# Kernel optimization log

Hardware: AMD Instinct MI355X
Metric: run time of the kernel (lower is better)

Reference implementation:

```python
import jax, jax.numpy as jnp
import numpy as np

D_MODEL = 1024


def setup_inputs() -> dict:
    key = jax.random.key(0)
    ks = jax.random.split(key, 11)
    B, S, D = 4, 2048, D_MODEL
    scale = 1.0 / np.sqrt(D)
    inp = {
        "query": jax.random.normal(ks[0], (B, S, D), dtype=jnp.float32),
        "key": jax.random.normal(ks[1], (B, S, D), dtype=jnp.float32),
        "value": jax.random.normal(ks[2], (B, S, D), dtype=jnp.float32),
        # nn.Linear weights stored torch-style as [out, in]; y = x @ W.T + b
        "Wq": jax.random.normal(ks[3], (D, D), dtype=jnp.float32) * scale,
        "bq": jnp.zeros((D,), dtype=jnp.float32),
        "Wk": jax.random.normal(ks[4], (D, D), dtype=jnp.float32) * scale,
        "bk": jnp.zeros((D,), dtype=jnp.float32),
        "Wv": jax.random.normal(ks[5], (D, D), dtype=jnp.float32) * scale,
        "bv": jnp.zeros((D,), dtype=jnp.float32),
        "Wo": jax.random.normal(ks[6], (D, D), dtype=jnp.float32) * scale,
        "bo": jnp.zeros((D,), dtype=jnp.float32),
    }
    return inp


def reference(query, key, value, Wq, bq, Wk, bk, Wv, bv, Wo, bo):
    d_model = query.shape[-1]
    q = jnp.einsum("bsd,ed->bse", query, Wq) + bq  # q_proj
    k = jnp.einsum("bsd,ed->bse", key, Wk) + bk    # k_proj
    v = jnp.einsum("bsd,ed->bse", value, Wv) + bv  # v_proj
    # scores scaled by sqrt(d_model) (single head: full d_model, per original code)
    scores = jnp.einsum("bqe,bke->bqk", q, k) / jnp.sqrt(jnp.asarray(d_model, q.dtype))
    attn = jax.nn.softmax(scores, axis=-1)
    # dropout is identity in eval mode
    out = jnp.einsum("bqk,bke->bqe", attn, v)
    out = jnp.einsum("bqe,fe->bqf", out, Wo) + bo  # out_proj
    return out
```

## Files before the change

kernel.cpp:

```cpp
#include <hip/hip_runtime.h>
#include <stdint.h>


typedef __bf16  bf16x8 __attribute__((ext_vector_type(8)));
typedef float   f32x4  __attribute__((ext_vector_type(4)));
typedef unsigned int u32x4 __attribute__((ext_vector_type(4)));

__device__ __forceinline__ unsigned short bf16_rne(float f) {
  unsigned int u = __builtin_bit_cast(unsigned int, f);
  u += 0x7FFFu + ((u >> 16) & 1u);
  return (unsigned short)(u >> 16);
}
__device__ __forceinline__ unsigned int pack2(float a, float b) {
  return (unsigned int)bf16_rne(a) | ((unsigned int)bf16_rne(b) << 16);
}
__device__ __forceinline__ void async16(const unsigned short* g, unsigned short* l) {
  __builtin_amdgcn_global_load_lds(
      (const __attribute__((address_space(1))) unsigned int*)g,
      (__attribute__((address_space(3))) unsigned int*)l,
      16, 0, 0);
}

#define FENCE() asm volatile("" ::: "memory")
#define BAR()   __builtin_amdgcn_s_barrier()

#define MFMA_ __builtin_amdgcn_mfma_f32_16x16x32_bf16

#define T1_REMAP() \
  const int nx   = gridDim.x, ny = gridDim.y; \
  const int nwg  = nx * ny * gridDim.z; \
  const int orig = (blockIdx.z * ny + blockIdx.y) * nx + blockIdx.x; \
  const int xcd  = orig & 7, loc = orig >> 3; \
  const int qq   = nwg >> 3, rr = nwg & 7; \
  const int w    = (xcd < rr ? xcd * (qq + 1) : rr * (qq + 1) + (xcd - rr) * qq) + loc; \
  const int bxi  = w % nx; \
  const int byi  = (w / nx) % ny; \
  const int bzi  = w / (nx * ny);

template<int OUT_F32>
__global__ __launch_bounds__(512, 1) void gemm256(
    const unsigned short* __restrict__ A, const unsigned short* __restrict__ B,
    void* __restrict__ Cp,
    int K, int lda, int ldb, int ldc,
    long sAz, long sBz, long sCz, long sBiasZ,
    float scale, const float* __restrict__ bias, int bias_mode)
{
  __shared__ unsigned short lds[2 * 32768];

  T1_REMAP();

  const int tid  = threadIdx.x;
  const int lane = tid & 63;
  const int wid  = tid >> 6;
  const int bm   = byi * 256;
  const int bn   = bxi * 256;
  const long z   = bzi;

  const unsigned short* Az = A + z * sAz;
  const unsigned short* Bz = B + z * sBz;

  const int wm  = wid >> 2;
  const int wn  = wid & 3;
  const int al  = lane & 15;
  const int ah  = lane >> 4;
  const int al7 = lane & 7;

  const int swz = ((lane & 7) ^ ((lane >> 3) & 7)) << 3;
  const unsigned short* Apt = Az + (long)(bm + wid * 32 + (lane >> 3)) * lda + swz;
  const unsigned short* Bpt = Bz + (long)(bn + wid * 32 + (lane >> 3)) * ldb + swz;
  const long a8 = (long)lda * 8, b8 = (long)ldb * 8;

#define SALL(kt, stg) { \
    const unsigned short* pa_ = Apt + ((long)(kt) << 6); \
    const unsigned short* pb_ = Bpt + ((long)(kt) << 6); \
    async16(pa_,          (stg) + wid * 2048);        \
    async16(pa_ + a8,     (stg) + wid * 2048 + 512);  \
    async16(pa_ + 2 * a8, (stg) + wid * 2048 + 1024); \
    async16(pa_ + 3 * a8, (stg) + wid * 2048 + 1536); \
    async16(pb_,          (stg) + 16384 + wid * 2048);        \
    async16(pb_ + b8,     (stg) + 16384 + wid * 2048 + 512);  \
    async16(pb_ + 2 * b8, (stg) + 16384 + wid * 2048 + 1024); \
    async16(pb_ + 3 * b8, (stg) + 16384 + wid * 2048 + 1536); }

#define LDA2(v0, v1, mm) { const int r_ = (wm * 128 + (mm) * 16 + al) * 64; \
    v0 = *(const bf16x8*)&as[r_ + ((ah ^ al7) << 3)]; \
    v1 = *(const bf16x8*)&as[r_ + (((4 | ah) ^ al7) << 3)]; }
#define LDB2(v0, v1, nn) { const int r_ = (wn * 64 + (nn) * 16 + al) * 64; \
    v0 = *(const bf16x8*)&bs[r_ + ((ah ^ al7) << 3)]; \
    v1 = *(const bf16x8*)&bs[r_ + (((4 | ah) ^ al7) << 3)]; }
#define MM2(mi, ni, av0, av1, bv0, bv1) { \
    acc[mi][ni] = MFMA_(av0, bv0, acc[mi][ni], 0, 0, 0); \
    acc[mi][ni] = MFMA_(av1, bv1, acc[mi][ni], 0, 0, 0); }

  f32x4 acc[8][4] = {};
  const int nkt = K >> 6;

  SALL(0, lds);

  int cur = 0;
  for (int t = 0; t < nkt; ++t) {
    asm volatile("s_waitcnt vmcnt(0)" ::: "memory");
    BAR(); FENCE();

    const unsigned short* as  = lds + cur * 32768;
    const unsigned short* bs  = as + 16384;
    unsigned short*       stg = lds + (cur ^ 1) * 32768;

    if (t + 1 < nkt) SALL(t + 1, stg);

    bf16x8 a0k0, a0k1, a1k0, a1k1, a2k0, a2k1, a3k0, a3k1;
    bf16x8 b0k0, b0k1, b1k0, b1k1, b2k0, b2k1, b3k0, b3k1;

    LDA2(a0k0, a0k1, 0); LDA2(a1k0, a1k1, 1); LDA2(a2k0, a2k1, 2); LDA2(a3k0, a3k1, 3);
    LDB2(b0k0, b0k1, 0); LDB2(b1k0, b1k1, 1);
    FENCE(); BAR();
    __builtin_amdgcn_s_setprio(1);
    MM2(0,0, a0k0,a0k1, b0k0,b0k1); MM2(1,0, a1k0,a1k1, b0k0,b0k1);
    MM2(2,0, a2k0,a2k1, b0k0,b0k1); MM2(3,0, a3k0,a3k1, b0k0,b0k1);
    MM2(0,1, a0k0,a0k1, b1k0,b1k1); MM2(1,1, a1k0,a1k1, b1k0,b1k1);
    MM2(2,1, a2k0,a2k1, b1k0,b1k1); MM2(3,1, a3k0,a3k1, b1k0,b1k1);
    __builtin_amdgcn_s_setprio(0);
    BAR(); FENCE();

    LDB2(b2k0, b2k1, 2); LDB2(b3k0, b3k1, 3);
    FENCE(); BAR();
    __builtin_amdgcn_s_setprio(1);
    MM2(0,2, a0k0,a0k1, b2k0,b2k1); MM2(1,2, a1k0,a1k1, b2k0,b2k1);
    MM2(2,2, a2k0,a2k1, b2k0,b2k1); MM2(3,2, a3k0,a3k1, b2k0,b2k1);
    MM2(0,3, a0k0,a0k1, b3k0,b3k1); MM2(1,3, a1k0,a1k1, b3k0,b3k1);
    MM2(2,3, a2k0,a2k1, b3k0,b3k1); MM2(3,3, a3k0,a3k1, b3k0,b3k1);
    __builtin_amdgcn_s_setprio(0);
    BAR(); FENCE();

    LDA2(a0k0, a0k1, 4); LDA2(a1k0, a1k1, 5); LDA2(a2k0, a2k1, 6); LDA2(a3k0, a3k1, 7);
    FENCE(); BAR();
    __builtin_amdgcn_s_setprio(1);
    MM2(4,0, a0k0,a0k1, b0k0,b0k1); MM2(5,0, a1k0,a1k1, b0k0,b0k1);
    MM2(6,0, a2k0,a2k1, b0k0,b0k1); MM2(7,0, a3k0,a3k1, b0k0,b0k1);
    MM2(4,1, a0k0,a0k1, b1k0,b1k1); MM2(5,1, a1k0,a1k1, b1k0,b1k1);
    MM2(6,1, a2k0,a2k1, b1k0,b1k1); MM2(7,1, a3k0,a3k1, b1k0,b1k1);
    __builtin_amdgcn_s_setprio(0);
    BAR(); FENCE();

    __builtin_amdgcn_s_setprio(1);
    MM2(4,2, a0k0,a0k1, b2k0,b2k1); MM2(5,2, a1k0,a1k1, b2k0,b2k1);
    MM2(6,2, a2k0,a2k1, b2k0,b2k1); MM2(7,2, a3k0,a3k1, b2k0,b2k1);
    MM2(4,3, a0k0,a0k1, b3k0,b3k1); MM2(5,3, a1k0,a1k1, b3k0,b3k1);
    MM2(6,3, a2k0,a2k1, b3k0,b3k1); MM2(7,3, a3k0,a3k1, b3k0,b3k1);
    __builtin_amdgcn_s_setprio(0);

    cur ^= 1;
  }

  #pragma unroll
  for (int m = 0; m < 8; ++m) {
    #pragma unroll
    for (int n = 0; n < 4; ++n) {
      #pragma unroll
      for (int j = 0; j < 4; ++j) {
        const int grow = bm + wm * 128 + m * 16 + ah * 4 + j;
        const int gcol = bn + wn * 64 + n * 16 + al;
        float v = acc[m][n][j] * scale;
        if (bias_mode == 1)      v += bias[z * sBiasZ + gcol];
        else if (bias_mode == 2) v += bias[z * sBiasZ + grow];
        const long idx = z * sCz + (long)grow * ldc + gcol;
        if (OUT_F32) ((float*)Cp)[idx] = v;
        else         ((unsigned short*)Cp)[idx] = bf16_rne(v);
      }
    }
  }
}

template<int OUT_F32>
__global__ __launch_bounds__(512, 2) void gemm8(
    const unsigned short* __restrict__ A, const unsigned short* __restrict__ B,
    void* __restrict__ Cp,
    int K, int lda, int ldb, int ldc,
    long sAz, long sBz, long sCz, long sBiasZ,
    float scale, const float* __restrict__ bias, int bias_mode)
{
  __shared__ unsigned short lds[3 * 24576];

  T1_REMAP();

  const int tid  = threadIdx.x;
  const int lane = tid & 63;
  const int wid  = tid >> 6;
  const int bm   = byi * 256;
  const int bn   = bxi * 128;
  const long z   = bzi;

  const unsigned short* Az = A + z * sAz;
  const unsigned short* Bz = B + z * sBz;

  const int wr  = (wid >> 1) * 64;
  const int wc  = (wid & 1)  * 64;
  const int al  = lane & 15;
  const int ah  = lane >> 4;
  const int al7 = lane & 7;

  const int swz = ((lane & 7) ^ ((lane >> 3) & 7)) << 3;
  const unsigned short* Apt = Az + (long)(bm + wid * 32 + (lane >> 3)) * lda + swz;
  const unsigned short* Bpt = Bz + (long)(bn + wid * 16 + (lane >> 3)) * ldb + swz;
  const long a8 = (long)lda * 8, b8 = (long)ldb * 8;

  f32x4 acc[4][4] = {};
  const int nkt = K >> 6;

#define STAGE_A(kt, stg) { const unsigned short* a_ = Apt + ((long)(kt) << 6); \
    async16(a_,          (stg) + wid * 2048);        \
    async16(a_ + a8,     (stg) + wid * 2048 + 512);  \
    async16(a_ + 2 * a8, (stg) + wid * 2048 + 1024); \
    async16(a_ + 3 * a8, (stg) + wid * 2048 + 1536); }
#define STAGE_B(kt, stg) { const unsigned short* b_ = Bpt + ((long)(kt) << 6); \
    async16(b_,      (stg) + 16384 + wid * 1024); \
    async16(b_ + b8, (stg) + 16384 + wid * 1024 + 512); }

#define LDA_(m) { const int r_ = (wr + (m) * 16 + al) * 64; \
    af##m##0 = *(const bf16x8*)&as[r_ + ((ah ^ al7) << 3)]; \
    af##m##1 = *(const bf16x8*)&as[r_ + (((4 | ah) ^ al7) << 3)]; }
#define LDB_(n) { const int r_ = (wc + (n) * 16 + al) * 64; \
    bf##n##0 = *(const bf16x8*)&bs[r_ + ((ah ^ al7) << 3)]; \
    bf##n##1 = *(const bf16x8*)&bs[r_ + (((4 | ah) ^ al7) << 3)]; }
#define MM(m, n) { \
    acc[m][n] = MFMA_(af##m##0, bf##n##0, acc[m][n], 0, 0, 0); \
    acc[m][n] = MFMA_(af##m##1, bf##n##1, acc[m][n], 0, 0, 0); }

  STAGE_A(0, lds); STAGE_B(0, lds);
  STAGE_A(1, lds + 24576); STAGE_B(1, lds + 24576);

  int cur = 0;
  for (int t = 0; t < nkt; ++t) {
    const int stb  = (cur >= 1) ? cur - 1 : cur + 2;
    const bool more = (t + 2) < nkt;

    if (t + 1 < nkt) asm volatile("s_waitcnt vmcnt(6)" ::: "memory");
    else             asm volatile("s_waitcnt vmcnt(0)" ::: "memory");
    BAR(); FENCE();

    const unsigned short* as  = lds + cur * 24576;
    const unsigned short* bs  = as + 16384;
    unsigned short*       stg = lds + stb * 24576;

    bf16x8 af00, af01, af10, af11, af20, af21, af30, af31;
    bf16x8 bf00, bf01, bf10, bf11, bf20, bf21, bf30, bf31;

    LDA_(0); LDA_(1); LDA_(2); LDA_(3);
    LDB_(0); LDB_(1);
    if (more) STAGE_A(t + 2, stg);
    FENCE(); BAR();
    __builtin_amdgcn_s_setprio(1);
    MM(0,0); MM(1,0); MM(2,0); MM(3,0);
    MM(0,1); MM(1,1); MM(2,1); MM(3,1);
    __builtin_amdgcn_s_setprio(0);
    BAR(); FENCE();

    LDB_(2); LDB_(3);
    if (more) STAGE_B(t + 2, stg);
    FENCE(); BAR();
    __builtin_amdgcn_s_setprio(1);
    MM(0,2); MM(1,2); MM(2,2); MM(3,2);
    MM(0,3); MM(1,3); MM(2,3); MM(3,3);
    __builtin_amdgcn_s_setprio(0);
    BAR(); FENCE();

    cur = (cur == 2) ? 0 : cur + 1;
  }

  #pragma unroll
  for (int m = 0; m < 4; ++m) {
    #pragma unroll
    for (int n = 0; n < 4; ++n) {
      #pragma unroll
      for (int j = 0; j < 4; ++j) {
        const int grow = bm + wr + m * 16 + ah * 4 + j;
        const int gcol = bn + wc + n * 16 + al;
        float v = acc[m][n][j] * scale;
        if (bias_mode == 1)      v += bias[z * sBiasZ + gcol];
        else if (bias_mode == 2) v += bias[z * sBiasZ + grow];
        const long idx = z * sCz + (long)grow * ldc + gcol;
        if (OUT_F32) ((float*)Cp)[idx] = v;
        else         ((unsigned short*)Cp)[idx] = bf16_rne(v);
      }
    }
  }
}

__device__ __forceinline__ void cvt8(const float* in, unsigned short* out, long i) {
  f32x4 a = *(const f32x4*)(in + i * 8);
  f32x4 b = *(const f32x4*)(in + i * 8 + 4);
  u32x4 w;
  w[0] = pack2(a[0], a[1]); w[1] = pack2(a[2], a[3]);
  w[2] = pack2(b[0], b[1]); w[3] = pack2(b[2], b[3]);
  *(u32x4*)(out + i * 8) = w;
}

__global__ __launch_bounds__(256) void mega_cvt2(
    const float* __restrict__ wq, const float* __restrict__ wk,
    const float* __restrict__ wv, const float* __restrict__ wo,
    const float* __restrict__ query, const float* __restrict__ key_,
    const float* __restrict__ bq, const float* __restrict__ bk,
    unsigned short* __restrict__ Wb, unsigned short* __restrict__ qf,
    unsigned short* __restrict__ kf, float* __restrict__ bqk)
{
  const int b = blockIdx.x;
  if (b < 2048) {
    const long i = (long)(b & 511) * 256 + threadIdx.x;
    if (b < 512)        cvt8(wq, Wb,            i);
    else if (b < 1024)  cvt8(wk, Wb + 1048576,  i);
    else if (b < 1536)  cvt8(wv, Wb + 2097152,  i);
    else                cvt8(wo, Wb + 3145728,  i);
  } else if (b < 6144) {
    cvt8(query, qf, (long)(b - 2048) * 256 + threadIdx.x);
  } else if (b < 10240) {
    cvt8(key_,  kf, (long)(b - 6144) * 256 + threadIdx.x);
  } else {
    const int t = (b - 10240) * 256 + threadIdx.x;
    if (t < 1024) bqk[t] = bq[t];
    else          bqk[t] = bk[t - 1024];
  }
}

__global__ __launch_bounds__(256) void cvt_f32_bf16(
    const float* __restrict__ in, unsigned short* __restrict__ out, int n8)
{
  const int i = blockIdx.x * 256 + threadIdx.x;
  if (i >= n8) return;
  cvt8(in, out, i);
}

__global__ __launch_bounds__(256) void softmax_inplace(unsigned short* __restrict__ P) {
  const long row = blockIdx.x;
  unsigned short* pr = P + row * 2048;
  const int tid = threadIdx.x;

  u32x4 raw = *(const u32x4*)&pr[tid * 8];
  float s[8];
  #pragma unroll
  for (int i = 0; i < 4; ++i) {
    unsigned int u = raw[i];
    s[2 * i]     = __builtin_bit_cast(float, u << 16);
    s[2 * i + 1] = __builtin_bit_cast(float, u & 0xFFFF0000u);
  }
  float m = s[0];
  #pragma unroll
  for (int i = 1; i < 8; ++i) m = fmaxf(m, s[i]);
  #pragma unroll
  for (int off = 32; off >= 1; off >>= 1) m = fmaxf(m, __shfl_xor(m, off));

  __shared__ float redm[4], reds[4];
  const int wid = tid >> 6, lane = tid & 63;
  if (lane == 0) redm[wid] = m;
  __syncthreads();
  m = fmaxf(fmaxf(redm[0], redm[1]), fmaxf(redm[2], redm[3]));

  float e[8], sum = 0.f;
  #pragma unroll
  for (int i = 0; i < 8; ++i) { e[i] = __expf(s[i] - m); sum += e[i]; }
  #pragma unroll
  for (int off = 32; off >= 1; off >>= 1) sum += __shfl_xor(sum, off);
  if (lane == 0) reds[wid] = sum;
  __syncthreads();
  sum = reds[0] + reds[1] + reds[2] + reds[3];
  const float inv = 1.0f / sum;

  u32x4 outw;
  #pragma unroll
  for (int i = 0; i < 4; ++i) outw[i] = pack2(e[2 * i] * inv, e[2 * i + 1] * inv);
  *(u32x4*)&pr[tid * 8] = outw;
}

extern "C" void kernel_launch(void* const* d_in, const int* in_sizes, int n_in,
                              void* d_out, int out_size, void* d_ws, size_t ws_size,
                              hipStream_t stream) {
  const float* query = (const float*)d_in[0];
  const float* key_  = (const float*)d_in[1];
  const float* value = (const float*)d_in[2];
  const float* Wq    = (const float*)d_in[3];
  const float* bq    = (const float*)d_in[4];
  const float* Wk    = (const float*)d_in[5];
  const float* bk    = (const float*)d_in[6];
  const float* Wv    = (const float*)d_in[7];
  const float* bv    = (const float*)d_in[8];
  const float* Wo    = (const float*)d_in[9];
  const float* bo    = (const float*)d_in[10];

  unsigned short* ws = (unsigned short*)d_ws;
  unsigned short* qf = ws;
  unsigned short* kf = ws + 8388608;
  unsigned short* vf = ws;
  unsigned short* P  = ws;
  unsigned short* q  = ws + 16777216;
  unsigned short* vT = ws + 33554432;
  unsigned short* Wb = ws + 41943040;
  float*          bqk= (float*)(ws + 46137344);
  unsigned short* o  = q;

  const dim3 blk(256), blk8(512);

  mega_cvt2<<<dim3(10248), blk, 0, stream>>>(Wq, Wk, Wv, Wo, query, key_,
                                             bq, bk, Wb, qf, kf, bqk);

  gemm256<0><<<dim3(4, 32, 2), blk8, 0, stream>>>(qf, Wb, q,
      1024, 1024, 1024, 1024, 8388608L, 1048576L, 8388608L, 1024L, 1.0f, bqk, 1);

  cvt_f32_bf16<<<dim3(4096), blk, 0, stream>>>(value, vf, 1048576);

  gemm8<0><<<dim3(64, 4, 1), blk8, 0, stream>>>(Wb + 2097152, vf, vT,
      1024, 1024, 1024, 8192, 0L, 0L, 0L, 0L, 1.0f, bv, 2);

  gemm256<0><<<dim3(8, 8, 4), blk8, 0, stream>>>(q, q + 8388608, P,
      1024, 1024, 1024, 2048, 2097152L, 2097152L, 4194304L, 0L, 0.03125f, nullptr, 0);

  softmax_inplace<<<dim3(8192), blk, 0, stream>>>(P);

  gemm8<0><<<dim3(8, 8, 4), blk8, 0, stream>>>(P, vT, o,
      2048, 2048, 8192, 1024, 4194304L, 2048L, 2097152L, 0L, 1.0f, nullptr, 0);

  gemm8<1><<<dim3(8, 32, 1), blk8, 0, stream>>>(o, Wb + 3145728, d_out,
      1024, 1024, 1024, 1024, 0L, 0L, 0L, 0L, 1.0f, bo, 1);
}
```

Baseline: 236.3 us.

## Drop intra-loop barriers in GEMM main loops and fuse value conversion

```diff
diff --git a/kernel.cpp b/kernel.cpp
--- a/kernel.cpp
+++ b/kernel.cpp
@@ -38,7 +38,7 @@
   const int bzi  = w / (nx * ny);
 
 template<int OUT_F32>
-__global__ __launch_bounds__(512, 1) void gemm256(
+__global__ __launch_bounds__(512) void gemm256(
     const unsigned short* __restrict__ A, const unsigned short* __restrict__ B,
     void* __restrict__ Cp,
     int K, int lda, int ldb, int ldc,
@@ -112,42 +112,25 @@
     bf16x8 b0k0, b0k1, b1k0, b1k1, b2k0, b2k1, b3k0, b3k1;
 
     LDA2(a0k0, a0k1, 0); LDA2(a1k0, a1k1, 1); LDA2(a2k0, a2k1, 2); LDA2(a3k0, a3k1, 3);
-    LDB2(b0k0, b0k1, 0); LDB2(b1k0, b1k1, 1);
-    FENCE(); BAR();
-    __builtin_amdgcn_s_setprio(1);
+    LDB2(b0k0, b0k1, 0); LDB2(b1k0, b1k1, 1); LDB2(b2k0, b2k1, 2); LDB2(b3k0, b3k1, 3);
     MM2(0,0, a0k0,a0k1, b0k0,b0k1); MM2(1,0, a1k0,a1k1, b0k0,b0k1);
     MM2(2,0, a2k0,a2k1, b0k0,b0k1); MM2(3,0, a3k0,a3k1, b0k0,b0k1);
     MM2(0,1, a0k0,a0k1, b1k0,b1k1); MM2(1,1, a1k0,a1k1, b1k0,b1k1);
     MM2(2,1, a2k0,a2k1, b1k0,b1k1); MM2(3,1, a3k0,a3k1, b1k0,b1k1);
-    __builtin_amdgcn_s_setprio(0);
-    BAR(); FENCE();
-
-    LDB2(b2k0, b2k1, 2); LDB2(b3k0, b3k1, 3);
-    FENCE(); BAR();
-    __builtin_amdgcn_s_setprio(1);
     MM2(0,2, a0k0,a0k1, b2k0,b2k1); MM2(1,2, a1k0,a1k1, b2k0,b2k1);
     MM2(2,2, a2k0,a2k1, b2k0,b2k1); MM2(3,2, a3k0,a3k1, b2k0,b2k1);
     MM2(0,3, a0k0,a0k1, b3k0,b3k1); MM2(1,3, a1k0,a1k1, b3k0,b3k1);
     MM2(2,3, a2k0,a2k1, b3k0,b3k1); MM2(3,3, a3k0,a3k1, b3k0,b3k1);
-    __builtin_amdgcn_s_setprio(0);
-    BAR(); FENCE();
 
     LDA2(a0k0, a0k1, 4); LDA2(a1k0, a1k1, 5); LDA2(a2k0, a2k1, 6); LDA2(a3k0, a3k1, 7);
-    FENCE(); BAR();
-    __builtin_amdgcn_s_setprio(1);
     MM2(4,0, a0k0,a0k1, b0k0,b0k1); MM2(5,0, a1k0,a1k1, b0k0,b0k1);
     MM2(6,0, a2k0,a2k1, b0k0,b0k1); MM2(7,0, a3k0,a3k1, b0k0,b0k1);
     MM2(4,1, a0k0,a0k1, b1k0,b1k1); MM2(5,1, a1k0,a1k1, b1k0,b1k1);
     MM2(6,1, a2k0,a2k1, b1k0,b1k1); MM2(7,1, a3k0,a3k1, b1k0,b1k1);
-    __builtin_amdgcn_s_setprio(0);
-    BAR(); FENCE();
-
-    __builtin_amdgcn_s_setprio(1);
     MM2(4,2, a0k0,a0k1, b2k0,b2k1); MM2(5,2, a1k0,a1k1, b2k0,b2k1);
     MM2(6,2, a2k0,a2k1, b2k0,b2k1); MM2(7,2, a3k0,a3k1, b2k0,b2k1);
     MM2(4,3, a0k0,a0k1, b3k0,b3k1); MM2(5,3, a1k0,a1k1, b3k0,b3k1);
     MM2(6,3, a2k0,a2k1, b3k0,b3k1); MM2(7,3, a3k0,a3k1, b3k0,b3k1);
-    __builtin_amdgcn_s_setprio(0);
 
     cur ^= 1;
   }
@@ -172,7 +155,7 @@
 }
 
 template<int OUT_F32>
-__global__ __launch_bounds__(512, 2) void gemm8(
+__global__ __launch_bounds__(512) void gemm8(
     const unsigned short* __restrict__ A, const unsigned short* __restrict__ B,
     void* __restrict__ Cp,
     int K, int lda, int ldb, int ldc,
@@ -207,14 +190,15 @@
   f32x4 acc[4][4] = {};
   const int nkt = K >> 6;
 
-#define STAGE_A(kt, stg) { const unsigned short* a_ = Apt + ((long)(kt) << 6); \
+#define STAGE_AB(kt, stg) { \
+    const unsigned short* a_ = Apt + ((long)(kt) << 6); \
+    const unsigned short* b_ = Bpt + ((long)(kt) << 6); \
     async16(a_,          (stg) + wid * 2048);        \
     async16(a_ + a8,     (stg) + wid * 2048 + 512);  \
     async16(a_ + 2 * a8, (stg) + wid * 2048 + 1024); \
-    async16(a_ + 3 * a8, (stg) + wid * 2048 + 1536); }
-#define STAGE_B(kt, stg) { const unsigned short* b_ = Bpt + ((long)(kt) << 6); \
-    async16(b_,      (stg) + 16384 + wid * 1024); \
-    async16(b_ + b8, (stg) + 16384 + wid * 1024 + 512); }
+    async16(a_ + 3 * a8, (stg) + wid * 2048 + 1536); \
+    async16(b_,          (stg) + 16384 + wid * 1024); \
+    async16(b_ + b8,     (stg) + 16384 + wid * 1024 + 512); }
 
 #define LDA_(m) { const int r_ = (wr + (m) * 16 + al) * 64; \
     af##m##0 = *(const bf16x8*)&as[r_ + ((ah ^ al7) << 3)]; \
@@ -226,13 +210,12 @@
     acc[m][n] = MFMA_(af##m##0, bf##n##0, acc[m][n], 0, 0, 0); \
     acc[m][n] = MFMA_(af##m##1, bf##n##1, acc[m][n], 0, 0, 0); }
 
-  STAGE_A(0, lds); STAGE_B(0, lds);
-  STAGE_A(1, lds + 24576); STAGE_B(1, lds + 24576);
+  STAGE_AB(0, lds);
+  STAGE_AB(1, lds + 24576);
 
   int cur = 0;
   for (int t = 0; t < nkt; ++t) {
     const int stb  = (cur >= 1) ? cur - 1 : cur + 2;
-    const bool more = (t + 2) < nkt;
 
     if (t + 1 < nkt) asm volatile("s_waitcnt vmcnt(6)" ::: "memory");
     else             asm volatile("s_waitcnt vmcnt(0)" ::: "memory");
@@ -242,27 +225,17 @@
     const unsigned short* bs  = as + 16384;
     unsigned short*       stg = lds + stb * 24576;
 
+    if (t + 2 < nkt) STAGE_AB(t + 2, stg);
+
     bf16x8 af00, af01, af10, af11, af20, af21, af30, af31;
     bf16x8 bf00, bf01, bf10, bf11, bf20, bf21, bf30, bf31;
 
     LDA_(0); LDA_(1); LDA_(2); LDA_(3);
-    LDB_(0); LDB_(1);
-    if (more) STAGE_A(t + 2, stg);
-    FENCE(); BAR();
-    __builtin_amdgcn_s_setprio(1);
+    LDB_(0); LDB_(1); LDB_(2); LDB_(3);
     MM(0,0); MM(1,0); MM(2,0); MM(3,0);
     MM(0,1); MM(1,1); MM(2,1); MM(3,1);
-    __builtin_amdgcn_s_setprio(0);
-    BAR(); FENCE();
-
-    LDB_(2); LDB_(3);
-    if (more) STAGE_B(t + 2, stg);
-    FENCE(); BAR();
-    __builtin_amdgcn_s_setprio(1);
     MM(0,2); MM(1,2); MM(2,2); MM(3,2);
     MM(0,3); MM(1,3); MM(2,3); MM(3,3);
-    __builtin_amdgcn_s_setprio(0);
-    BAR(); FENCE();
 
     cur = (cur == 2) ? 0 : cur + 1;
   }
@@ -295,13 +268,15 @@
   *(u32x4*)(out + i * 8) = w;
 }
 
-__global__ __launch_bounds__(256) void mega_cvt2(
+__global__ __launch_bounds__(256) void mega_cvt3(
     const float* __restrict__ wq, const float* __restrict__ wk,
     const float* __restrict__ wv, const float* __restrict__ wo,
     const float* __restrict__ query, const float* __restrict__ key_,
+    const float* __restrict__ value,
     const float* __restrict__ bq, const float* __restrict__ bk,
     unsigned short* __restrict__ Wb, unsigned short* __restrict__ qf,
-    unsigned short* __restrict__ kf, float* __restrict__ bqk)
+    unsigned short* __restrict__ kf, unsigned short* __restrict__ vf,
+    float* __restrict__ bqk)
 {
   const int b = blockIdx.x;
   if (b < 2048) {
@@ -314,10 +289,12 @@
     cvt8(query, qf, (long)(b - 2048) * 256 + threadIdx.x);
   } else if (b < 10240) {
     cvt8(key_,  kf, (long)(b - 6144) * 256 + threadIdx.x);
-  } else {
+  } else if (b < 10248) {
     const int t = (b - 10240) * 256 + threadIdx.x;
     if (t < 1024) bqk[t] = bq[t];
     else          bqk[t] = bk[t - 1024];
+  } else {
+    cvt8(value, vf, (long)(b - 10248) * 256 + threadIdx.x);
   }
 }
 
@@ -388,7 +365,6 @@
   unsigned short* ws = (unsigned short*)d_ws;
   unsigned short* qf = ws;
   unsigned short* kf = ws + 8388608;
-  unsigned short* vf = ws;
   unsigned short* P  = ws;
   unsigned short* q  = ws + 16777216;
   unsigned short* vT = ws + 33554432;
@@ -396,15 +372,19 @@
   float*          bqk= (float*)(ws + 46137344);
   unsigned short* o  = q;
 
+  const bool par = ws_size >= (size_t)(46141440 + 8388608) * 2;
+  unsigned short* vf = par ? (ws + 46141440) : ws;
+
   const dim3 blk(256), blk8(512);
 
-  mega_cvt2<<<dim3(10248), blk, 0, stream>>>(Wq, Wk, Wv, Wo, query, key_,
-                                             bq, bk, Wb, qf, kf, bqk);
+  mega_cvt3<<<dim3(par ? 14344 : 10248), blk, 0, stream>>>(
+      Wq, Wk, Wv, Wo, query, key_, value, bq, bk, Wb, qf, kf, vf, bqk);
 
   gemm256<0><<<dim3(4, 32, 2), blk8, 0, stream>>>(qf, Wb, q,
       1024, 1024, 1024, 1024, 8388608L, 1048576L, 8388608L, 1024L, 1.0f, bqk, 1);
 
-  cvt_f32_bf16<<<dim3(4096), blk, 0, stream>>>(value, vf, 1048576);
+  if (!par)
+    cvt_f32_bf16<<<dim3(4096), blk, 0, stream>>>(value, vf, 1048576);
 
   gemm8<0><<<dim3(64, 4, 1), blk8, 0, stream>>>(Wb + 2097152, vf, vT,
       1024, 1024, 1024, 8192, 0L, 0L, 0L, 0L, 1.0f, bv, 2);
```

After: 226.0 us. -4.4%, faster.
